# Kernel tuning notes

Measured on AMD Instinct MI355X. Metric: run time of the kernel, lower is better.

Reference implementation:

```python
import jax, jax.numpy as jnp
import numpy as np

B = 256      # graph pairs
N = 256      # nodes per graph (uniform -> padding is a reshape)
DEG = 16     # avg degree
D = 32       # one_hot_dim
F1, F2, F3 = 128, 64, 64
T = 16       # tensor_neurons
BINS = 16
BOT = 16     # bottle_neck_neurons


def setup_inputs() -> dict:
    key = jax.random.key(0)
    ks = jax.random.split(key, 24)
    NT = B * N            # total nodes per side
    NE = B * N * DEG      # total directed edges per side
    x_q = jax.random.normal(ks[0], (NT, D), jnp.float32)
    x_c = jax.random.normal(ks[1], (NT, D), jnp.float32)
    edge_q = jax.random.randint(ks[2], (2, NE), 0, NT, jnp.int32)
    edge_c = jax.random.randint(ks[3], (2, NE), 0, NT, jnp.int32)
    qgraph_sizes = jnp.full((B,), N, jnp.int32)
    cgraph_sizes = jnp.full((B,), N, jnp.int32)

    def glorot(k, shape):
        fan = sum(shape[-2:]) if len(shape) >= 2 else shape[0] * 2
        return jax.random.uniform(k, shape, jnp.float32, -1.0, 1.0) * np.sqrt(6.0 / fan)

    params = dict(
        W1=glorot(ks[4], (D, F1)), b1=jnp.zeros((F1,), jnp.float32),
        W2=glorot(ks[5], (F1, F2)), b2=jnp.zeros((F2,), jnp.float32),
        W3=glorot(ks[6], (F2, F3)), b3=jnp.zeros((F3,), jnp.float32),
        attn_w=glorot(ks[7], (F3, F3)),
        ntn_a_w=glorot(ks[8], (T, F3, F3)),
        ntn_b_w=glorot(ks[9], (2 * F3, T)),
        ntn_bias=glorot(ks[10], (T, 1)),
        fc1_w=glorot(ks[11], (T + BINS, BOT)), fc1_b=jnp.zeros((BOT,), jnp.float32),
        fc2_w=glorot(ks[12], (BOT, 1)), fc2_b=jnp.zeros((1,), jnp.float32),
    )
    return dict(x_q=x_q, edge_q=edge_q, x_c=x_c, edge_c=edge_c,
                qgraph_sizes=qgraph_sizes, cgraph_sizes=cgraph_sizes, **params)


def _gcn(x, src, dst, W, b):
    n = x.shape[0]
    h = x @ W
    loop = jnp.arange(n, dtype=src.dtype)
    s = jnp.concatenate([src, loop])
    d = jnp.concatenate([dst, loop])
    deg = jax.ops.segment_sum(jnp.ones(s.shape, h.dtype), d, num_segments=n)
    dinv = jnp.where(deg > 0, jax.lax.rsqrt(jnp.maximum(deg, 1.0)), 0.0)
    coef = (dinv[s] * dinv[d])[:, None]
    return jax.ops.segment_sum(h[s] * coef, d, num_segments=n) + b


def _gnn(x, ei, W1, b1, W2, b2, W3, b3):
    src, dst = ei[0], ei[1]
    h = jax.nn.relu(_gcn(x, src, dst, W1, b1))        # dropout is identity in eval
    h = jax.nn.relu(_gcn(h, src, dst, W2, b2))
    return _gcn(h, src, dst, W3, b3)                  # [B*N, F3]


def _att_pool(q, attn_w, sizes):
    # q: [B, N, F3]
    ctx = jnp.tanh((q.sum(axis=1) @ attn_w) / sizes.astype(q.dtype)[:, None])  # [B, F3]
    sig = jax.nn.sigmoid(jnp.einsum('bnf,bf->bn', q, ctx))                      # [B, N]
    return jnp.einsum('bnf,bn->bf', q, sig)                                     # [B, F3]


def _pair_hist(q, c):
    # per-pair histogram of q @ c^T with BINS bins over each pair's [min, max]
    s = jax.lax.stop_gradient(jnp.einsum('bnf,bmf->bnm', q, c))  # [B, N, N]
    mn = s.min(axis=(1, 2), keepdims=True)
    mx = s.max(axis=(1, 2), keepdims=True)
    idx = jnp.clip(jnp.floor((s - mn) / jnp.maximum(mx - mn, 1e-12) * BINS),
                   0, BINS - 1).astype(jnp.int32)
    gid = (idx + jnp.arange(B, dtype=jnp.int32)[:, None, None] * BINS).reshape(-1)
    h = jax.ops.segment_sum(jnp.ones(gid.shape, jnp.float32), gid,
                            num_segments=B * BINS).reshape(B, BINS)
    return h / h.sum(axis=1, keepdims=True)


def reference(x_q, edge_q, x_c, edge_c, qgraph_sizes, cgraph_sizes,
              W1, b1, W2, b2, W3, b3, attn_w, ntn_a_w, ntn_b_w, ntn_bias,
              fc1_w, fc1_b, fc2_w, fc2_b):
    q = _gnn(x_q, edge_q, W1, b1, W2, b2, W3, b3).reshape(B, N, F3)
    c = _gnn(x_c, edge_c, W1, b1, W2, b2, W3, b3).reshape(B, N, F3)
    e1 = _att_pool(q, attn_w, qgraph_sizes)
    e2 = _att_pool(c, attn_w, cgraph_sizes)
    ntn = (jnp.einsum('bi,tij,bj->bt', e1, ntn_a_w, e2)
           + jnp.concatenate([e1, e2], axis=-1) @ ntn_b_w
           + ntn_bias[:, 0])
    scores = jax.nn.relu(ntn)                                   # [B, T]
    hist = _pair_hist(q, c)                                     # [B, BINS]
    scores = jnp.concatenate([scores, hist], axis=1)
    scores = jax.nn.relu(scores @ fc1_w + fc1_b)
    p = jax.nn.sigmoid(scores @ fc2_w + fc2_b)[:, 0]            # [B]
    ged = -0.5 * (qgraph_sizes + cgraph_sizes).astype(p.dtype) * jnp.log(p)
    return ged
```

## Files before the change

### kernel.cpp

```cpp
#include <hip/hip_runtime.h>
#include <hip/hip_bf16.h>
#include <math.h>

#define BB 256
#define NN 256
#define NT (BB*NN)
#define NT2 (2*NT)
#define NE (NT*16)
#define DD 32
#define F1C 128
#define F2C 64
#define F3C 64
#define TT 16
#define BINS 16

#define NBUCK 256
#define BSHIFT 9
#define BNODES 512
#define BCAP 10240
#define EPB 4096

typedef __attribute__((ext_vector_type(8))) short short8;
typedef __attribute__((ext_vector_type(4))) float f32x4;
typedef __attribute__((ext_vector_type(2))) float f32x2;

__device__ inline float b2f(ushort u) { return __uint_as_float(((uint)u) << 16); }
__device__ inline ushort f2b(float f) {
    uint u = __float_as_uint(f);
    return (ushort)((u + 0x7fffu + ((u >> 16) & 1u)) >> 16);
}
__device__ inline float clamp8(float v) { return fminf(fmaxf(v, -448.0f), 448.0f); }
__device__ inline uchar f2f8(float v) {
    int r = __builtin_amdgcn_cvt_pk_fp8_f32(clamp8(v), 0.0f, 0, false);
    return (uchar)(r & 0xff);
}
__device__ inline void f8x8_acc(uint2 w, float* acc) {
    f32x2 p;
    p = __builtin_amdgcn_cvt_pk_f32_fp8(w.x, false); acc[0] += p.x; acc[1] += p.y;
    p = __builtin_amdgcn_cvt_pk_f32_fp8(w.x, true);  acc[2] += p.x; acc[3] += p.y;
    p = __builtin_amdgcn_cvt_pk_f32_fp8(w.y, false); acc[4] += p.x; acc[5] += p.y;
    p = __builtin_amdgcn_cvt_pk_f32_fp8(w.y, true);  acc[6] += p.x; acc[7] += p.y;
}
__device__ inline uint2 f8x8_pack(const float* v) {
    uint2 r;
    r.x = (uint)__builtin_amdgcn_cvt_pk_fp8_f32(clamp8(v[0]), clamp8(v[1]), 0, false);
    r.x = (uint)__builtin_amdgcn_cvt_pk_fp8_f32(clamp8(v[2]), clamp8(v[3]), (int)r.x, true);
    r.y = (uint)__builtin_amdgcn_cvt_pk_fp8_f32(clamp8(v[4]), clamp8(v[5]), 0, false);
    r.y = (uint)__builtin_amdgcn_cvt_pk_fp8_f32(clamp8(v[6]), clamp8(v[7]), (int)r.y, true);
    return r;
}

__global__ __launch_bounds__(256) void zero_k(int* __restrict__ gcount) {
    gcount[threadIdx.x] = 0;
}

__global__ __launch_bounds__(256) void p1cvt_k(const int* __restrict__ eq, const int* __restrict__ ec,
                                               uint* __restrict__ staged, int* __restrict__ gcount,
                                               const float* __restrict__ W1, const float* __restrict__ W2,
                                               const float* __restrict__ W3, ushort* __restrict__ Wt1,
                                               ushort* __restrict__ Wt2, uchar* __restrict__ Wt3f8) {
    int t = threadIdx.x;
    if (blockIdx.x < 512) {
        __shared__ uint s_pk[EPB];
        __shared__ int s_cnt[NBUCK];
        __shared__ int s_off[NBUCK];
        __shared__ int s_base[NBUCK];
        __shared__ int s_gb[NBUCK];
        bool sideB = blockIdx.x >= 256;
        const int* edge = sideB ? ec : eq;
        int off = sideB ? NT : 0;
        int e0 = (blockIdx.x & 255) * EPB;
        s_cnt[t] = 0;
        __syncthreads();
        uint pk[16]; int bk[16];
#pragma unroll
        for (int j = 0; j < 16; j++) {
            int e = e0 + j * 256 + t;
            int s = edge[e] + off;
            int d = edge[NE + e] + off;
            bk[j] = d >> BSHIFT;
            pk[j] = ((uint)s << BSHIFT) | (uint)(d & (BNODES - 1));
            atomicAdd(&s_cnt[bk[j]], 1);
        }
        __syncthreads();
        s_off[t] = s_cnt[t];
        __syncthreads();
        for (int o = 1; o < NBUCK; o <<= 1) {
            int x = (t >= o) ? s_off[t - o] : 0;
            __syncthreads();
            s_off[t] += x;
            __syncthreads();
        }
        {
            int ex = s_off[t] - s_cnt[t];
            s_base[t] = ex;
            s_off[t] = ex;
            s_gb[t] = atomicAdd(&gcount[t], s_cnt[t]);
        }
        __syncthreads();
#pragma unroll
        for (int j = 0; j < 16; j++) {
            int pos = atomicAdd(&s_off[bk[j]], 1);
            s_pk[pos] = pk[j];
        }
        __syncthreads();
        int w = t >> 6, l = t & 63;
        int bsel = l >> 4, l16 = l & 15;
        for (int pb = w; pb < NBUCK / 4; pb += 4) {
            int bkt = pb * 4 + bsel;
            int n = s_cnt[bkt], st = s_base[bkt], gb = s_gb[bkt];
            if (gb + n > BCAP) n = max(0, BCAP - gb);
            for (int i = l16; i < n; i += 16)
                staged[bkt * BCAP + gb + i] = s_pk[st + i];
        }
    } else {
        int i = (blockIdx.x - 512) * 256 + t;
        if (i < DD * F1C)  { int k = i / F1C, n = i % F1C; Wt1[n * DD + k]  = f2b(W1[i]); }
        if (i < F1C * F2C) { int k = i / F2C, n = i % F2C; Wt2[n * F1C + k] = f2b(W2[i]); }
        if (i < F2C * F3C) { int k = i / F3C, n = i % F3C; Wt3f8[n * F2C + k] = f2f8(W3[i]); }
    }
}

__global__ __launch_bounds__(256) void csr_p2_k(const uint* __restrict__ staged, const int* __restrict__ gcount,
                                                int* __restrict__ rp, int* __restrict__ indeg,
                                                float* __restrict__ dinv, int* __restrict__ ep,
                                                const float* __restrict__ xq, const float* __restrict__ xc,
                                                ushort* __restrict__ xb) {
    int b = blockIdx.x;
    int t = threadIdx.x;
    __shared__ int cnt[BNODES];
    __shared__ int fl[BNODES];
    __shared__ int wsum[256];
    __shared__ int gsc[NBUCK];
    __shared__ float sdv[BNODES];
    cnt[t] = 0; cnt[t + 256] = 0;
    gsc[t] = min(gcount[t], BCAP);
    __syncthreads();
    for (int off = 1; off < NBUCK; off <<= 1) {
        int x = (t >= off) ? gsc[t - off] : 0;
        __syncthreads();
        gsc[t] += x;
        __syncthreads();
    }
    int gbase = (b == 0) ? 0 : gsc[b - 1];
    int n = min(gcount[b], BCAP);
    const uint* sb = staged + (size_t)b * BCAP;
    int i = t;
    for (; i + 768 < n; i += 1024) {
        uint p0 = sb[i];
        uint p1 = sb[i + 256];
        uint p2 = sb[i + 512];
        uint p3 = sb[i + 768];
        atomicAdd(&cnt[p0 & (BNODES - 1)], 1);
        atomicAdd(&cnt[p1 & (BNODES - 1)], 1);
        atomicAdd(&cnt[p2 & (BNODES - 1)], 1);
        atomicAdd(&cnt[p3 & (BNODES - 1)], 1);
    }
    for (; i < n; i += 256)
        atomicAdd(&cnt[sb[i] & (BNODES - 1)], 1);
    __syncthreads();
    int base2 = t * 2;
    int c0 = cnt[base2], c1 = cnt[base2 + 1];
    int s2 = c0 + c1;
    wsum[t] = s2;
    __syncthreads();
    for (int off = 1; off < 256; off <<= 1) {
        int x = (t >= off) ? wsum[t - off] : 0;
        __syncthreads();
        wsum[t] += x;
        __syncthreads();
    }
    int p = gbase + wsum[t] - s2;
    int v0 = b * BNODES + base2;
    float d0 = rsqrtf((float)(c0 + 1));
    float d1 = rsqrtf((float)(c1 + 1));
    rp[v0] = p;          fl[base2] = p;
    indeg[v0] = c0;      dinv[v0] = d0;      sdv[base2] = d0;
    p += c0;
    rp[v0 + 1] = p;      fl[base2 + 1] = p;
    indeg[v0 + 1] = c1;  dinv[v0 + 1] = d1;  sdv[base2 + 1] = d1;
    __syncthreads();
    i = t;
    for (; i + 768 < n; i += 1024) {
        uint p0 = sb[i];
        uint p1 = sb[i + 256];
        uint p2 = sb[i + 512];
        uint p3 = sb[i + 768];
        ep[atomicAdd(&fl[p0 & (BNODES - 1)], 1)] = (int)(p0 >> BSHIFT);
        ep[atomicAdd(&fl[p1 & (BNODES - 1)], 1)] = (int)(p1 >> BSHIFT);
        ep[atomicAdd(&fl[p2 & (BNODES - 1)], 1)] = (int)(p2 >> BSHIFT);
        ep[atomicAdd(&fl[p3 & (BNODES - 1)], 1)] = (int)(p3 >> BSHIFT);
    }
    for (; i < n; i += 256) {
        uint pk = sb[i];
        ep[atomicAdd(&fl[pk & (BNODES - 1)], 1)] = (int)(pk >> BSHIFT);
    }
    {
        const float* xs = (b < 128) ? (xq + (size_t)b * BNODES * DD)
                                    : (xc + ((size_t)b * BNODES - NT) * DD);
        ushort* xd = xb + (size_t)b * BNODES * DD;
        for (int g = t; g < BNODES * DD / 4; g += 256) {
            int r = g >> 3;
            float4 v = ((const float4*)xs)[g];
            float dv = sdv[r];
            ushort4 o;
            o.x = f2b(v.x * dv); o.y = f2b(v.y * dv);
            o.z = f2b(v.z * dv); o.w = f2b(v.w * dv);
            ((ushort4*)xd)[g] = o;
        }
    }
}

__global__ __launch_bounds__(256) void agg_bf_k(const ushort* __restrict__ in, const int* __restrict__ rp,
                                                const int* __restrict__ indeg, const int* __restrict__ ep,
                                                const float* __restrict__ dinv,
                                                ushort* __restrict__ out) {
    int g = threadIdx.x >> 2;
    int l = threadIdx.x & 3;
    int v = blockIdx.x * 64 + g;
    float dv = dinv[v];
    short8 rs = *(const short8*)(in + (size_t)v * 32 + l * 8);
    float acc[8];
#pragma unroll
    for (int j = 0; j < 8; j++) acc[j] = b2f((ushort)rs[j]);
    int start = rp[v];
    int cnt   = indeg[v];
    int i = 0;
    for (; i + 4 <= cnt; i += 4) {
        int s0 = ep[start + i];
        int s1 = ep[start + i + 1];
        int s2 = ep[start + i + 2];
        int s3 = ep[start + i + 3];
        short8 r0 = *(const short8*)(in + (size_t)s0 * 32 + l * 8);
        short8 r1 = *(const short8*)(in + (size_t)s1 * 32 + l * 8);
        short8 r2 = *(const short8*)(in + (size_t)s2 * 32 + l * 8);
        short8 r3 = *(const short8*)(in + (size_t)s3 * 32 + l * 8);
#pragma unroll
        for (int j = 0; j < 8; j++) {
            acc[j] += b2f((ushort)r0[j]);
            acc[j] += b2f((ushort)r1[j]);
            acc[j] += b2f((ushort)r2[j]);
            acc[j] += b2f((ushort)r3[j]);
        }
    }
    for (; i < cnt; i++) {
        int s0 = ep[start + i];
        short8 r0 = *(const short8*)(in + (size_t)s0 * 32 + l * 8);
#pragma unroll
        for (int j = 0; j < 8; j++) acc[j] += b2f((ushort)r0[j]);
    }
    short8 o;
#pragma unroll
    for (int j = 0; j < 8; j++) o[j] = (short)f2b(dv * acc[j]);
    *(short8*)(out + (size_t)v * 32 + l * 8) = o;
}

template<bool OUT_BF16, bool BIAS, bool RELU>
__global__ __launch_bounds__(256) void agg_f8_k(const uchar* __restrict__ in, const int* __restrict__ rp,
                                                const int* __restrict__ indeg, const int* __restrict__ ep,
                                                const float* __restrict__ dinv,
                                                const float* __restrict__ bias, void* __restrict__ outp) {
    int g = threadIdx.x >> 3;
    int l = threadIdx.x & 7;
    int v = blockIdx.x * 32 + g;
    float dv = dinv[v];
    float acc[8] = {0, 0, 0, 0, 0, 0, 0, 0};
    f8x8_acc(*(const uint2*)(in + (size_t)v * 64 + l * 8), acc);
    int start = rp[v];
    int cnt   = indeg[v];
    int i = 0;
    for (; i + 8 <= cnt; i += 8) {
        int sx[8];
#pragma unroll
        for (int j = 0; j < 8; j++) sx[j] = ep[start + i + j];
        uint2 gx[8];
#pragma unroll
        for (int j = 0; j < 8; j++) gx[j] = *(const uint2*)(in + (size_t)sx[j] * 64 + l * 8);
#pragma unroll
        for (int j = 0; j < 8; j++) f8x8_acc(gx[j], acc);
    }
    for (; i + 4 <= cnt; i += 4) {
        int s0 = ep[start + i];
        int s1 = ep[start + i + 1];
        int s2 = ep[start + i + 2];
        int s3 = ep[start + i + 3];
        uint2 g0 = *(const uint2*)(in + (size_t)s0 * 64 + l * 8);
        uint2 g1 = *(const uint2*)(in + (size_t)s1 * 64 + l * 8);
        uint2 g2 = *(const uint2*)(in + (size_t)s2 * 64 + l * 8);
        uint2 g3 = *(const uint2*)(in + (size_t)s3 * 64 + l * 8);
        f8x8_acc(g0, acc); f8x8_acc(g1, acc); f8x8_acc(g2, acc); f8x8_acc(g3, acc);
    }
    for (; i < cnt; i++) {
        int s0 = ep[start + i];
        f8x8_acc(*(const uint2*)(in + (size_t)s0 * 64 + l * 8), acc);
    }
#pragma unroll
    for (int j = 0; j < 8; j++) {
        float x = dv * acc[j];
        if (BIAS) x += bias[l * 8 + j];
        if (RELU) x = fmaxf(x, 0.0f);
        acc[j] = x;
    }
    if (OUT_BF16) {
        short8 o;
#pragma unroll
        for (int j = 0; j < 8; j++) o[j] = (short)f2b(acc[j]);
        *(short8*)((ushort*)outp + (size_t)v * 64 + l * 8) = o;
    } else {
        *(uint2*)((uchar*)outp + (size_t)v * 64 + l * 8) = f8x8_pack(acc);
    }
}

__global__ __launch_bounds__(256) void gemm12_k(const ushort* __restrict__ xa,
                                                const ushort* __restrict__ Wt1,
                                                const float* __restrict__ b1,
                                                const ushort* __restrict__ Wt2,
                                                const float* __restrict__ dinv,
                                                uchar* __restrict__ h8a) {
    __shared__ ushort s_h1[128][136];
    int w = threadIdx.x >> 6, lane = threadIdx.x & 63;
    int r16 = lane & 15, quad = lane >> 4, koff = quad * 8;
    size_t rows0 = (size_t)blockIdx.x * 128;

    short8 af1[2];
#pragma unroll
    for (int mt = 0; mt < 2; mt++)
        af1[mt] = *(const short8*)(xa + (rows0 + (w * 2 + mt) * 16 + r16) * 32 + koff);
#pragma unroll
    for (int nt = 0; nt < 8; nt++) {
        short8 bfr = *(const short8*)(Wt1 + (size_t)(nt * 16 + r16) * 32 + koff);
        f32x4 acc[2] = {{0.f,0.f,0.f,0.f},{0.f,0.f,0.f,0.f}};
        acc[0] = __builtin_amdgcn_mfma_f32_16x16x32_bf16(af1[0], bfr, acc[0], 0, 0, 0);
        acc[1] = __builtin_amdgcn_mfma_f32_16x16x32_bf16(af1[1], bfr, acc[1], 0, 0, 0);
        int col = nt * 16 + r16;
        float bc = b1[col];
#pragma unroll
        for (int mt = 0; mt < 2; mt++)
#pragma unroll
            for (int r = 0; r < 4; r++) {
                int rl = (w * 2 + mt) * 16 + quad * 4 + r;
                s_h1[rl][col] = f2b(fmaxf(acc[mt][r] + bc, 0.0f));
            }
    }
    __syncthreads();

    short8 af2[4][2];
#pragma unroll
    for (int kc = 0; kc < 4; kc++)
#pragma unroll
        for (int mt = 0; mt < 2; mt++)
            af2[kc][mt] = *(const short8*)&s_h1[(w * 2 + mt) * 16 + r16][kc * 32 + koff];
    float dvr[2][4];
#pragma unroll
    for (int mt = 0; mt < 2; mt++)
#pragma unroll
        for (int r = 0; r < 4; r++)
            dvr[mt][r] = dinv[rows0 + (w * 2 + mt) * 16 + quad * 4 + r];
#pragma unroll
    for (int nt = 0; nt < 4; nt++) {
        f32x4 acc[2] = {{0.f,0.f,0.f,0.f},{0.f,0.f,0.f,0.f}};
#pragma unroll
        for (int kc = 0; kc < 4; kc++) {
            short8 bfr = *(const short8*)(Wt2 + (size_t)(nt * 16 + r16) * 128 + kc * 32 + koff);
            acc[0] = __builtin_amdgcn_mfma_f32_16x16x32_bf16(af2[kc][0], bfr, acc[0], 0, 0, 0);
            acc[1] = __builtin_amdgcn_mfma_f32_16x16x32_bf16(af2[kc][1], bfr, acc[1], 0, 0, 0);
        }
#pragma unroll
        for (int mt = 0; mt < 2; mt++)
#pragma unroll
            for (int r = 0; r < 4; r++) {
                size_t row = rows0 + (w * 2 + mt) * 16 + quad * 4 + r;
                int col = nt * 16 + r16;
                h8a[row * 64 + col] = f2f8(acc[mt][r] * dvr[mt][r]);
            }
    }
}

__global__ __launch_bounds__(256) void gemm_f8_k(const uchar* __restrict__ A8,
                                                 const uchar* __restrict__ Wt8,
                                                 const float* __restrict__ dinv,
                                                 uchar* __restrict__ out8) {
    int w = threadIdx.x >> 6, lane = threadIdx.x & 63;
    int r16 = lane & 15, koff = (lane >> 4) * 8;
    size_t rows0 = (size_t)blockIdx.x * 128;

    long af[2][2];
#pragma unroll
    for (int kc = 0; kc < 2; kc++)
#pragma unroll
        for (int mt = 0; mt < 2; mt++)
            af[kc][mt] = *(const long*)(A8 + (rows0 + (w * 2 + mt) * 16 + r16) * 64 + kc * 32 + koff);

    float dvr[2][4];
#pragma unroll
    for (int mt = 0; mt < 2; mt++)
#pragma unroll
        for (int r = 0; r < 4; r++)
            dvr[mt][r] = dinv[rows0 + (w * 2 + mt) * 16 + (lane >> 4) * 4 + r];

#pragma unroll
    for (int nt = 0; nt < 4; nt++) {
        f32x4 acc[2] = {{0.f,0.f,0.f,0.f},{0.f,0.f,0.f,0.f}};
#pragma unroll
        for (int kc = 0; kc < 2; kc++) {
            long b = *(const long*)(Wt8 + (size_t)(nt * 16 + r16) * 64 + kc * 32 + koff);
            acc[0] = __builtin_amdgcn_mfma_f32_16x16x32_fp8_fp8(af[kc][0], b, acc[0], 0, 0, 0);
            acc[1] = __builtin_amdgcn_mfma_f32_16x16x32_fp8_fp8(af[kc][1], b, acc[1], 0, 0, 0);
        }
#pragma unroll
        for (int mt = 0; mt < 2; mt++) {
#pragma unroll
            for (int r = 0; r < 4; r++) {
                size_t row = rows0 + (w * 2 + mt) * 16 + (lane >> 4) * 4 + r;
                int col = nt * 16 + (lane & 15);
                out8[row * 64 + col] = f2f8(acc[mt][r] * dvr[mt][r]);
            }
        }
    }
}

__global__ __launch_bounds__(256) void pool_hist_k(const ushort* __restrict__ fin,
                                                   const int* __restrict__ qsz, const int* __restrict__ csz,
                                                   const float* __restrict__ attn_w,
                                                   float* __restrict__ e_out, float* __restrict__ histp) {
    __shared__ float smemf[17472];
    int t = threadIdx.x;
    if (blockIdx.x < 512) {
        int b = blockIdx.x & 255;
        bool is_c = blockIdx.x >= BB;
        const ushort* emb = fin + (size_t)blockIdx.x * NN * F3C;
        float size = (float)((is_c ? csz : qsz)[b]);
        float* eo = e_out + (is_c ? BB * F3C : 0) + b * F3C;
        float (*s_emb)[F3C + 1] = (float(*)[F3C + 1])smemf;
        float* s_red = smemf + 256 * 65;
        float* s_sq  = s_red + 256;
        float* s_ctx = s_sq + 64;
        float* s_sig = s_ctx + 64;
        int f = t & 63;
        int w = t >> 6;
#pragma unroll
        for (int it = 0; it < 8; it++) {
            int idx = it * 2048 + t * 8;
            int row = idx >> 6, f0 = idx & 63;
            short8 v = *(const short8*)(emb + idx);
#pragma unroll
            for (int j = 0; j < 8; j++) s_emb[row][f0 + j] = b2f((ushort)v[j]);
        }
        __syncthreads();
        float psum = 0.0f;
#pragma unroll 8
        for (int i2 = 0; i2 < 64; i2++) psum += s_emb[w * 64 + i2][f];
        s_red[w * 64 + f] = psum;
        __syncthreads();
        if (w == 0) {
            s_sq[f] = s_red[f] + s_red[64 + f] + s_red[128 + f] + s_red[192 + f];
            float acc = 0.0f;
            for (int k = 0; k < 64; k++) acc += s_sq[k] * attn_w[k * 64 + f];
            s_ctx[f] = tanhf(acc / size);
        }
        __syncthreads();
        {
            float acc = 0.0f;
#pragma unroll 8
            for (int k = 0; k < 64; k++) acc += s_emb[t][k] * s_ctx[k];
            s_sig[t] = 1.0f / (1.0f + expf(-acc));
        }
        __syncthreads();
        float eacc = 0.0f;
#pragma unroll 8
        for (int i = 0; i < 64; i++) {
            int n = w * 64 + i;
            eacc += s_sig[n] * s_emb[n][f];
        }
        s_red[w * 64 + f] = eacc;
        __syncthreads();
        if (w == 0) eo[f] = s_red[f] + s_red[64 + f] + s_red[128 + f] + s_red[192 + f];
    } else {
        int b = blockIdx.x - 512;
        const ushort* qb = fin + (size_t)b * NN * 64;
        const ushort* cb = fin + (size_t)(NT + b * NN) * 64;
        int lane = t & 63;
        int w = t >> 6;
        int r16 = lane & 15, koff = (lane >> 4) * 8;
        ushort (*cb_s)[72] = (ushort(*)[72])smemf;
        int* h = (int*)(smemf + 9216);
        int* hp = h + 16 * 256;
        float* smn = (float*)(hp + 256);
        float* smx = smn + 4;
        float* s_sc = smx + 4;

#pragma unroll
        for (int it = 0; it < 8; it++) {
            int idx = it * 2048 + t * 8;
            int row = idx >> 6, f0 = idx & 63;
            *(short8*)&cb_s[row][f0] = *(const short8*)(cb + idx);
        }
        short8 a[4][2];
#pragma unroll
        for (int i = 0; i < 4; i++) {
            int row = (w * 4 + i) * 16 + r16;
#pragma unroll
            for (int kk = 0; kk < 2; kk++)
                a[i][kk] = *(const short8*)(qb + row * 64 + kk * 32 + koff);
        }
        __syncthreads();
        float mn = 1e30f, mx = -1e30f;
        for (int mt = 0; mt < 16; mt++) {
            int crow = mt * 16 + r16;
            short8 b0 = *(const short8*)&cb_s[crow][koff];
            short8 b1 = *(const short8*)&cb_s[crow][32 + koff];
#pragma unroll
            for (int i = 0; i < 4; i++) {
                f32x4 acc = {0.0f, 0.0f, 0.0f, 0.0f};
                acc = __builtin_amdgcn_mfma_f32_16x16x32_bf16(a[i][0], b0, acc, 0, 0, 0);
                acc = __builtin_amdgcn_mfma_f32_16x16x32_bf16(a[i][1], b1, acc, 0, 0, 0);
                mn = fminf(mn, fminf(fminf(acc[0], acc[1]), fminf(acc[2], acc[3])));
                mx = fmaxf(mx, fmaxf(fmaxf(acc[0], acc[1]), fmaxf(acc[2], acc[3])));
            }
        }
        for (int off = 32; off; off >>= 1) {
            mn = fminf(mn, __shfl_xor(mn, off, 64));
            mx = fmaxf(mx, __shfl_xor(mx, off, 64));
        }
        if (lane == 0) { smn[w] = mn; smx[w] = mx; }
        __syncthreads();
        if (t == 0) {
            float m0 = fminf(fminf(smn[0], smn[1]), fminf(smn[2], smn[3]));
            float m1 = fmaxf(fmaxf(smx[0], smx[1]), fmaxf(smx[2], smx[3]));
            s_sc[0] = m0;
            s_sc[1] = 16.0f / fmaxf(m1 - m0, 1e-12f);
        }
#pragma unroll
        for (int i = 0; i < 16; i++) h[i * 256 + t] = 0;
        __syncthreads();
        float bmn = s_sc[0], bscale = s_sc[1];
        for (int mt = 0; mt < 16; mt++) {
            int crow = mt * 16 + r16;
            short8 b0 = *(const short8*)&cb_s[crow][koff];
            short8 b1 = *(const short8*)&cb_s[crow][32 + koff];
#pragma unroll
            for (int i = 0; i < 4; i++) {
                f32x4 acc = {0.0f, 0.0f, 0.0f, 0.0f};
                acc = __builtin_amdgcn_mfma_f32_16x16x32_bf16(a[i][0], b0, acc, 0, 0, 0);
                acc = __builtin_amdgcn_mfma_f32_16x16x32_bf16(a[i][1], b1, acc, 0, 0, 0);
#pragma unroll
                for (int r = 0; r < 4; r++) {
                    int bin = (int)floorf((acc[r] - bmn) * bscale);
                    bin = min(max(bin, 0), 15);
                    h[bin * 256 + t] += 1;
                }
            }
        }
        __syncthreads();
        int bb = t >> 4, part = t & 15;
        int sum = 0;
#pragma unroll
        for (int j = 0; j < 16; j++) sum += h[bb * 256 + part * 16 + j];
        hp[bb * 16 + part] = sum;
        __syncthreads();
        if (t < 16) {
            int s = 0;
#pragma unroll
            for (int j = 0; j < 16; j++) s += hp[t * 16 + j];
            histp[b * 16 + t] = (float)s;
        }
    }
}

__global__ __launch_bounds__(256) void ntn_final_k(const float* __restrict__ e, const float* __restrict__ A,
                                                   const float* __restrict__ bw, const float* __restrict__ bias,
                                                   const float* __restrict__ histp,
                                                   const float* __restrict__ fc1w, const float* __restrict__ fc1b,
                                                   const float* __restrict__ fc2w, const float* __restrict__ fc2b,
                                                   const int* __restrict__ qsz, const int* __restrict__ csz,
                                                   float* __restrict__ out) {
    int b = blockIdx.x;
    int t = threadIdx.x;
    int lane = t & 63, w = t >> 6;
    __shared__ float s_e1[64], s_e2[64];
    __shared__ float s_ntn[16];
    __shared__ float s_s[32];
    __shared__ float s_a[16];
    if (t < 64) s_e1[t] = e[b * 64 + t];
    else if (t < 128) s_e2[t - 64] = e[BB * 64 + b * 64 + (t - 64)];
    __syncthreads();
#pragma unroll
    for (int r = 0; r < 4; r++) {
        int idx = t + r * 256;
        const float4* Ar = (const float4*)(A + (size_t)idx * 64);
        float acc = 0.0f;
#pragma unroll
        for (int j = 0; j < 16; j++) {
            float4 a4 = Ar[j];
            acc += a4.x * s_e2[4 * j] + a4.y * s_e2[4 * j + 1]
                 + a4.z * s_e2[4 * j + 2] + a4.w * s_e2[4 * j + 3];
        }
        float p = s_e1[lane] * acc;
        for (int off = 32; off; off >>= 1) p += __shfl_xor(p, off, 64);
        if (lane == 0) s_ntn[w + 4 * r] = p;
    }
    __syncthreads();
    if (t < 16) {
        float acc = s_ntn[t] + bias[t];
        for (int k = 0; k < 64; k++) acc += s_e1[k] * bw[k * 16 + t];
        for (int k = 0; k < 64; k++) acc += s_e2[k] * bw[(64 + k) * 16 + t];
        s_s[t] = fmaxf(acc, 0.0f);
        s_s[16 + t] = histp[b * 16 + t] * (1.0f / 65536.0f);
    }
    __syncthreads();
    if (t < 16) {
        float a = fc1b[t];
        for (int k = 0; k < 32; k++) a += s_s[k] * fc1w[k * 16 + t];
        s_a[t] = fmaxf(a, 0.0f);
    }
    __syncthreads();
    if (t == 0) {
        float z = fc2b[0];
        for (int j = 0; j < 16; j++) z += s_a[j] * fc2w[j];
        float nz = -z;
        float sp = (nz > 20.0f) ? nz : log1pf(expf(nz));
        out[b] = 0.5f * (float)(qsz[b] + csz[b]) * sp;
    }
}

extern "C" void kernel_launch(void* const* d_in, const int* in_sizes, int n_in,
                              void* d_out, int out_size, void* d_ws, size_t ws_size,
                              hipStream_t stream) {
    const float* x_q    = (const float*)d_in[0];
    const int*   edge_q = (const int*)d_in[1];
    const float* x_c    = (const float*)d_in[2];
    const int*   edge_c = (const int*)d_in[3];
    const int*   qsz    = (const int*)d_in[4];
    const int*   csz    = (const int*)d_in[5];
    const float* W1 = (const float*)d_in[6];
    const float* b1 = (const float*)d_in[7];
    const float* W2 = (const float*)d_in[8];
    const float* b2 = (const float*)d_in[9];
    const float* W3 = (const float*)d_in[10];
    const float* b3 = (const float*)d_in[11];
    const float* attn_w  = (const float*)d_in[12];
    const float* ntn_a   = (const float*)d_in[13];
    const float* ntn_b   = (const float*)d_in[14];
    const float* ntn_bias= (const float*)d_in[15];
    const float* fc1w = (const float*)d_in[16];
    const float* fc1b = (const float*)d_in[17];
    const float* fc2w = (const float*)d_in[18];
    const float* fc2b = (const float*)d_in[19];
    float* out = (float*)d_out;

    char* w = (char*)d_ws;
    auto alloc = [&](size_t bytes) -> void* {
        void* p = (void*)w;
        w += (bytes + 255) & ~(size_t)255;
        return p;
    };
    int*    rp     = (int*)alloc((size_t)NT2 * 4);
    int*    indeg  = (int*)alloc((size_t)NT2 * 4);
    float*  dinv   = (float*)alloc((size_t)NT2 * 4);
    int*    gcount = (int*)alloc(NBUCK * 4);
    uint*   staged = (uint*)alloc((size_t)NBUCK * BCAP * 4);
    int*    ep     = (int*)alloc((size_t)2 * NE * 4);
    ushort* xb     = (ushort*)alloc((size_t)NT2 * 32 * 2);
    ushort* xa     = (ushort*)alloc((size_t)NT2 * 32 * 2);
    uchar*  h8a    = (uchar*)alloc((size_t)NT2 * 64);
    uchar*  h8b    = (uchar*)alloc((size_t)NT2 * 64);
    ushort* fin    = (ushort*)alloc((size_t)NT2 * 64 * 2);
    ushort* Wt1    = (ushort*)alloc((size_t)DD * F1C * 2);
    ushort* Wt2    = (ushort*)alloc((size_t)F1C * F2C * 2);
    uchar*  Wt3f8  = (uchar*)alloc((size_t)F2C * F3C);
    float*  e12    = (float*)alloc(2 * BB * 64 * 4);
    float*  histp  = (float*)alloc(256 * 16 * 4);

    zero_k<<<1, 256, 0, stream>>>(gcount);
    p1cvt_k<<<512 + 32, 256, 0, stream>>>(edge_q, edge_c, staged, gcount,
                                          W1, W2, W3, Wt1, Wt2, Wt3f8);
    csr_p2_k<<<NBUCK, 256, 0, stream>>>(staged, gcount, rp, indeg, dinv, ep,
                                        x_q, x_c, xb);

    agg_bf_k<<<NT2 / 64, 256, 0, stream>>>(xb, rp, indeg, ep, dinv, xa);
    gemm12_k<<<NT2 / 128, 256, 0, stream>>>(xa, Wt1, b1, Wt2, dinv, h8a);
    agg_f8_k<false, true, true><<<NT2 / 32, 256, 0, stream>>>(h8a, rp, indeg, ep, dinv, b2, h8b);
    gemm_f8_k<<<NT2 / 128, 256, 0, stream>>>(h8b, Wt3f8, dinv, h8a);
    agg_f8_k<true, true, false><<<NT2 / 32, 256, 0, stream>>>(h8a, rp, indeg, ep, dinv, b3, fin);

    pool_hist_k<<<768, 256, 0, stream>>>(fin, qsz, csz, attn_w, e12, histp);
    ntn_final_k<<<BB, 256, 0, stream>>>(e12, ntn_a, ntn_b, ntn_bias, histp,
                                        fc1w, fc1b, fc2w, fc2b, qsz, csz, out);
}
```

Baseline: 282.6 us.

## Widen pool/hist kernel to 1024 threads and use ushort histogram counters

```diff
diff --git a/kernel.cpp b/kernel.cpp
--- a/kernel.cpp
+++ b/kernel.cpp
@@ -419,12 +419,14 @@
     }
 }
 
-__global__ __launch_bounds__(256) void pool_hist_k(const ushort* __restrict__ fin,
-                                                   const int* __restrict__ qsz, const int* __restrict__ csz,
-                                                   const float* __restrict__ attn_w,
-                                                   float* __restrict__ e_out, float* __restrict__ histp) {
-    __shared__ float smemf[17472];
+__global__ __launch_bounds__(1024) void pool_hist_k(const ushort* __restrict__ fin,
+                                                    const int* __restrict__ qsz, const int* __restrict__ csz,
+                                                    const float* __restrict__ attn_w,
+                                                    float* __restrict__ e_out, float* __restrict__ histp) {
+    __shared__ float smemf[18944];
     int t = threadIdx.x;
+    int f = t & 63;
+    int w = t >> 6;
     if (blockIdx.x < 512) {
         int b = blockIdx.x & 255;
         bool is_c = blockIdx.x >= BB;
@@ -432,15 +434,13 @@
         float size = (float)((is_c ? csz : qsz)[b]);
         float* eo = e_out + (is_c ? BB * F3C : 0) + b * F3C;
         float (*s_emb)[F3C + 1] = (float(*)[F3C + 1])smemf;
-        float* s_red = smemf + 256 * 65;
-        float* s_sq  = s_red + 256;
+        float* s_red = smemf + 16640;
+        float* s_sq  = s_red + 1024;
         float* s_ctx = s_sq + 64;
         float* s_sig = s_ctx + 64;
-        int f = t & 63;
-        int w = t >> 6;
-#pragma unroll
-        for (int it = 0; it < 8; it++) {
-            int idx = it * 2048 + t * 8;
+#pragma unroll
+        for (int it = 0; it < 2; it++) {
+            int idx = it * 8192 + t * 8;
             int row = idx >> 6, f0 = idx & 63;
             short8 v = *(const short8*)(emb + idx);
 #pragma unroll
@@ -449,17 +449,20 @@
         __syncthreads();
         float psum = 0.0f;
 #pragma unroll 8
-        for (int i2 = 0; i2 < 64; i2++) psum += s_emb[w * 64 + i2][f];
+        for (int i2 = 0; i2 < 16; i2++) psum += s_emb[w * 16 + i2][f];
         s_red[w * 64 + f] = psum;
         __syncthreads();
         if (w == 0) {
-            s_sq[f] = s_red[f] + s_red[64 + f] + s_red[128 + f] + s_red[192 + f];
+            float s = 0.0f;
+#pragma unroll
+            for (int j = 0; j < 16; j++) s += s_red[j * 64 + f];
+            s_sq[f] = s;
             float acc = 0.0f;
             for (int k = 0; k < 64; k++) acc += s_sq[k] * attn_w[k * 64 + f];
             s_ctx[f] = tanhf(acc / size);
         }
         __syncthreads();
-        {
+        if (t < 256) {
             float acc = 0.0f;
 #pragma unroll 8
             for (int k = 0; k < 64; k++) acc += s_emb[t][k] * s_ctx[k];
@@ -468,40 +471,43 @@
         __syncthreads();
         float eacc = 0.0f;
 #pragma unroll 8
-        for (int i = 0; i < 64; i++) {
-            int n = w * 64 + i;
+        for (int i = 0; i < 16; i++) {
+            int n = w * 16 + i;
             eacc += s_sig[n] * s_emb[n][f];
         }
         s_red[w * 64 + f] = eacc;
         __syncthreads();
-        if (w == 0) eo[f] = s_red[f] + s_red[64 + f] + s_red[128 + f] + s_red[192 + f];
+        if (w == 0) {
+            float s = 0.0f;
+#pragma unroll
+            for (int j = 0; j < 16; j++) s += s_red[j * 64 + f];
+            eo[f] = s;
+        }
     } else {
         int b = blockIdx.x - 512;
         const ushort* qb = fin + (size_t)b * NN * 64;
         const ushort* cb = fin + (size_t)(NT + b * NN) * 64;
         int lane = t & 63;
-        int w = t >> 6;
         int r16 = lane & 15, koff = (lane >> 4) * 8;
         ushort (*cb_s)[72] = (ushort(*)[72])smemf;
-        int* h = (int*)(smemf + 9216);
-        int* hp = h + 16 * 256;
-        float* smn = (float*)(hp + 256);
-        float* smx = smn + 4;
-        float* s_sc = smx + 4;
-
-#pragma unroll
-        for (int it = 0; it < 8; it++) {
-            int idx = it * 2048 + t * 8;
+        ushort* h = (ushort*)(smemf + 9216);
+        int* hp = (int*)(smemf + 9216 + 8192);
+        float* smn = smemf + 9216 + 8192 + 1024;
+        float* smx = smn + 16;
+        float* s_sc = smx + 16;
+
+#pragma unroll
+        for (int it = 0; it < 2; it++) {
+            int idx = it * 8192 + t * 8;
             int row = idx >> 6, f0 = idx & 63;
             *(short8*)&cb_s[row][f0] = *(const short8*)(cb + idx);
         }
-        short8 a[4][2];
-#pragma unroll
-        for (int i = 0; i < 4; i++) {
-            int row = (w * 4 + i) * 16 + r16;
+        short8 a[2];
+        {
+            int qrow = w * 16 + r16;
 #pragma unroll
             for (int kk = 0; kk < 2; kk++)
-                a[i][kk] = *(const short8*)(qb + row * 64 + kk * 32 + koff);
+                a[kk] = *(const short8*)(qb + qrow * 64 + kk * 32 + koff);
         }
         __syncthreads();
         float mn = 1e30f, mx = -1e30f;
@@ -509,14 +515,11 @@
             int crow = mt * 16 + r16;
             short8 b0 = *(const short8*)&cb_s[crow][koff];
             short8 b1 = *(const short8*)&cb_s[crow][32 + koff];
-#pragma unroll
-            for (int i = 0; i < 4; i++) {
-                f32x4 acc = {0.0f, 0.0f, 0.0f, 0.0f};
-                acc = __builtin_amdgcn_mfma_f32_16x16x32_bf16(a[i][0], b0, acc, 0, 0, 0);
-                acc = __builtin_amdgcn_mfma_f32_16x16x32_bf16(a[i][1], b1, acc, 0, 0, 0);
-                mn = fminf(mn, fminf(fminf(acc[0], acc[1]), fminf(acc[2], acc[3])));
-                mx = fmaxf(mx, fmaxf(fmaxf(acc[0], acc[1]), fmaxf(acc[2], acc[3])));
-            }
+            f32x4 acc = {0.0f, 0.0f, 0.0f, 0.0f};
+            acc = __builtin_amdgcn_mfma_f32_16x16x32_bf16(a[0], b0, acc, 0, 0, 0);
+            acc = __builtin_amdgcn_mfma_f32_16x16x32_bf16(a[1], b1, acc, 0, 0, 0);
+            mn = fminf(mn, fminf(fminf(acc[0], acc[1]), fminf(acc[2], acc[3])));
+            mx = fmaxf(mx, fmaxf(fmaxf(acc[0], acc[1]), fmaxf(acc[2], acc[3])));
         }
         for (int off = 32; off; off >>= 1) {
             mn = fminf(mn, __shfl_xor(mn, off, 64));
@@ -525,43 +528,44 @@
         if (lane == 0) { smn[w] = mn; smx[w] = mx; }
         __syncthreads();
         if (t == 0) {
-            float m0 = fminf(fminf(smn[0], smn[1]), fminf(smn[2], smn[3]));
-            float m1 = fmaxf(fmaxf(smx[0], smx[1]), fmaxf(smx[2], smx[3]));
+            float m0 = smn[0], m1 = smx[0];
+#pragma unroll
+            for (int j = 1; j < 16; j++) {
+                m0 = fminf(m0, smn[j]);
+                m1 = fmaxf(m1, smx[j]);
+            }
             s_sc[0] = m0;
             s_sc[1] = 16.0f / fmaxf(m1 - m0, 1e-12f);
         }
 #pragma unroll
-        for (int i = 0; i < 16; i++) h[i * 256 + t] = 0;
+        for (int i = 0; i < 16; i++) h[i * 1024 + t] = 0;
         __syncthreads();
         float bmn = s_sc[0], bscale = s_sc[1];
         for (int mt = 0; mt < 16; mt++) {
             int crow = mt * 16 + r16;
             short8 b0 = *(const short8*)&cb_s[crow][koff];
             short8 b1 = *(const short8*)&cb_s[crow][32 + koff];
-#pragma unroll
-            for (int i = 0; i < 4; i++) {
-                f32x4 acc = {0.0f, 0.0f, 0.0f, 0.0f};
-                acc = __builtin_amdgcn_mfma_f32_16x16x32_bf16(a[i][0], b0, acc, 0, 0, 0);
-                acc = __builtin_amdgcn_mfma_f32_16x16x32_bf16(a[i][1], b1, acc, 0, 0, 0);
-#pragma unroll
-                for (int r = 0; r < 4; r++) {
-                    int bin = (int)floorf((acc[r] - bmn) * bscale);
-                    bin = min(max(bin, 0), 15);
-                    h[bin * 256 + t] += 1;
-                }
+            f32x4 acc = {0.0f, 0.0f, 0.0f, 0.0f};
+            acc = __builtin_amdgcn_mfma_f32_16x16x32_bf16(a[0], b0, acc, 0, 0, 0);
+            acc = __builtin_amdgcn_mfma_f32_16x16x32_bf16(a[1], b1, acc, 0, 0, 0);
+#pragma unroll
+            for (int r = 0; r < 4; r++) {
+                int bin = (int)floorf((acc[r] - bmn) * bscale);
+                bin = min(max(bin, 0), 15);
+                h[bin * 1024 + t] += 1;
             }
         }
         __syncthreads();
-        int bb = t >> 4, part = t & 15;
+        int bb = t >> 6, part = t & 63;
         int sum = 0;
 #pragma unroll
-        for (int j = 0; j < 16; j++) sum += h[bb * 256 + part * 16 + j];
-        hp[bb * 16 + part] = sum;
+        for (int j = 0; j < 16; j++) sum += (int)h[bb * 1024 + part * 16 + j];
+        hp[bb * 64 + part] = sum;
         __syncthreads();
         if (t < 16) {
             int s = 0;
 #pragma unroll
-            for (int j = 0; j < 16; j++) s += hp[t * 16 + j];
+            for (int j = 0; j < 64; j++) s += hp[t * 64 + j];
             histp[b * 16 + t] = (float)s;
         }
     }
@@ -683,7 +687,7 @@
     gemm_f8_k<<<NT2 / 128, 256, 0, stream>>>(h8b, Wt3f8, dinv, h8a);
     agg_f8_k<true, true, false><<<NT2 / 32, 256, 0, stream>>>(h8a, rp, indeg, ep, dinv, b3, fin);
 
-    pool_hist_k<<<768, 256, 0, stream>>>(fin, qsz, csz, attn_w, e12, histp);
+    pool_hist_k<<<768, 1024, 0, stream>>>(fin, qsz, csz, attn_w, e12, histp);
     ntn_final_k<<<BB, 256, 0, stream>>>(e12, ntn_a, ntn_b, ntn_bias, histp,
                                         fc1w, fc1b, fc2w, fc2b, qsz, csz, out);
 }
```

After: 278.1 us. Within noise of the previous version (-1.6%).
